# Optimization experiments

Hardware: AMD Instinct MI355X
Metric: run time of the kernel (lower is better)

Reference implementation:

```python
import jax, jax.numpy as jnp
import numpy as np
import math

T, B, H, L = 512, 64, 512, 2
STDV = 1.0 / math.sqrt(H)


def setup_inputs() -> dict:
    key = jax.random.key(0)
    ks = jax.random.split(key, 16)
    u = lambda k, shape: jax.random.uniform(k, shape, jnp.float32, -STDV, STDV)
    inp = {
        "x": jax.random.normal(ks[0], (T, B, H), jnp.float32),
        "init_states": jax.random.normal(ks[1], (L, B, H), jnp.float32),
        # stacked per-layer GRU cell parameters (input_size == hidden_size)
        "w_ir": u(ks[2], (L, H, H)), "w_hr": u(ks[3], (L, H, H)),
        "w_iz": u(ks[4], (L, H, H)), "w_hz": u(ks[5], (L, H, H)),
        "w_in": u(ks[6], (L, H, H)), "w_hn": u(ks[7], (L, H, H)),
        "b_ir": u(ks[8], (L, H)), "b_hr": u(ks[9], (L, H)),
        "b_iz": u(ks[10], (L, H)), "b_hz": u(ks[11], (L, H)),
        "b_in": u(ks[12], (L, H)), "b_hn": u(ks[13], (L, H)),
    }
    return inp


def _gru_layer(inputs, h0, w_ir, w_hr, w_iz, w_hz, w_in, w_hn,
               b_ir, b_hr, b_iz, b_hz, b_in, b_hn):
    # inputs: [T, B, H]; h0: [B, H]
    def step(h, xt):
        r = jax.nn.sigmoid(xt @ w_ir + b_ir + h @ w_hr + b_hr)
        z = jax.nn.sigmoid(xt @ w_iz + b_iz + h @ w_hz + b_hz)
        n = jnp.tanh(xt @ w_in + b_in + r * (h @ w_hn + b_hn))
        h_new = (1.0 - z) * n + z * h
        return h_new, h_new
    h_last, hs = jax.lax.scan(step, h0, inputs)
    return hs, h_last  # [T, B, H], [B, H]


def reference(x, init_states, w_ir, w_hr, w_iz, w_hz, w_in, w_hn,
              b_ir, b_hr, b_iz, b_hz, b_in, b_hn):
    num_layers = w_ir.shape[0]
    inputs = x
    finals = []
    for l in range(num_layers):
        inputs, h_last = _gru_layer(
            inputs, init_states[l],
            w_ir[l], w_hr[l], w_iz[l], w_hz[l], w_in[l], w_hn[l],
            b_ir[l], b_hr[l], b_iz[l], b_hz[l], b_in[l], b_hn[l])
        finals.append(h_last)
    # (last-layer outputs over all timesteps [T,B,H], per-layer final hidden [L,B,H])
    return inputs, jnp.stack(finals, axis=0)
```

## Files before the change

kernel.cpp:

```cpp
#include <hip/hip_runtime.h>
#include <math.h>


typedef short bf16x8 __attribute__((ext_vector_type(8)));
typedef float f32x4 __attribute__((ext_vector_type(4)));

__device__ __forceinline__ unsigned short f2bf(float f) {
  unsigned u = __builtin_bit_cast(unsigned, f);
  return (unsigned short)((u + 0x7fff + ((u >> 16) & 1)) >> 16);
}
__device__ __forceinline__ unsigned long long ldq(const unsigned long long* p) {
  return __hip_atomic_load(p, __ATOMIC_RELAXED, __HIP_MEMORY_SCOPE_AGENT);
}
__device__ __forceinline__ void stq(unsigned long long* p,
                                    unsigned long long v) {
  __hip_atomic_store(p, v, __ATOMIC_RELAXED, __HIP_MEMORY_SCOPE_AGENT);
}

__device__ __forceinline__ int hchunk(int k, int b) {
  return ((b >> 4) * 16 + (k >> 5)) * 64 + ((k >> 3) & 3) * 16 + (b & 15);
}

__device__ __forceinline__ void grid_barrier(unsigned* bar, unsigned target) {
  __syncthreads();
  if (threadIdx.x == 0) {
    unsigned leaf = blockIdx.x & 7u;
    unsigned prev = __hip_atomic_fetch_add(bar + leaf * 32, 1u,
                                           __ATOMIC_RELAXED,
                                           __HIP_MEMORY_SCOPE_AGENT);
    bool done = false;
    if ((prev & 15u) == 15u) {
      unsigned p2 = __hip_atomic_fetch_add(bar + 256, 1u, __ATOMIC_RELAXED,
                                           __HIP_MEMORY_SCOPE_AGENT);
      if ((p2 & 7u) == 7u) {
        __hip_atomic_store(bar + 288, target, __ATOMIC_RELAXED,
                           __HIP_MEMORY_SCOPE_AGENT);
        done = true;
      }
    }
    if (!done) {
      while (__hip_atomic_load(bar + 288, __ATOMIC_RELAXED,
                               __HIP_MEMORY_SCOPE_AGENT) < target) {
        __builtin_amdgcn_s_sleep(1);
      }
    }
  }
  __syncthreads();
}

__global__ void gru_prep_h(const float* __restrict__ init,
                           unsigned short* __restrict__ h0buf,
                           unsigned short* __restrict__ h1buf,
                           unsigned* __restrict__ bar) {
  int l = blockIdx.x >> 6;
  int idx = (blockIdx.x & 63) * 512 + threadIdx.x;
  int k = idx >> 6, b = idx & 63;
  unsigned short v = f2bf(init[(size_t)l * 32768 + b * 512 + k]);
  unsigned short* dst = (l == 0) ? h0buf : h1buf;
  dst[hchunk(k, b) * 8 + (k & 7)] = v;
  if (blockIdx.x == 0 && threadIdx.x < 512) bar[threadIdx.x] = 0u;
}

__global__ void gru_xprep(const float* __restrict__ x,
                          unsigned short* __restrict__ xbf) {
  int t = blockIdx.x;
#pragma unroll
  for (int it = 0; it < 8; ++it) {
    int ck = it * 512 + threadIdx.x;
    int b = (ck >> 10) * 16 + (ck & 15);
    int k0 = ((ck >> 6) & 15) * 32 + ((ck >> 4) & 3) * 8;
    const float* src = x + ((size_t)t * 64 + b) * 512 + k0;
    float4 v0 = *(const float4*)(src);
    float4 v1 = *(const float4*)(src + 4);
    unsigned short o[8] = {f2bf(v0.x), f2bf(v0.y), f2bf(v0.z), f2bf(v0.w),
                           f2bf(v1.x), f2bf(v1.y), f2bf(v1.z), f2bf(v1.w)};
    *(uint4*)(xbf + (size_t)t * 32768 + ck * 8) = *(const uint4*)o;
  }
}

__global__ void gru_wimg(const float* __restrict__ Wir,
                         const float* __restrict__ Wiz,
                         const float* __restrict__ Win,
                         const float* __restrict__ Whr,
                         const float* __restrict__ Whz,
                         const float* __restrict__ Whn,
                         unsigned short* __restrict__ wX,
                         unsigned short* __restrict__ wH) {
  int l = blockIdx.x >> 6, blk = blockIdx.x & 63;
  size_t base = ((size_t)l * 64 + blk) * 32 * 512;
  size_t wbase = (size_t)l * 512 * 512;
  for (int idx = threadIdx.x; idx < 16384; idx += 256) {
    int c = idx & 7, k = (idx >> 3) & 511, q = idx >> 12;
    int col = blk * 8 + c;
    int row = c * 4 + q;
    size_t we = wbase + (size_t)k * 512 + col;
    float vx = 0.f, vh = 0.f;
    if (q == 0) { vx = Wir[we]; vh = Whr[we]; }
    else if (q == 1) { vx = Wiz[we]; vh = Whz[we]; }
    else if (q == 2) { vx = Win[we]; }
    else { vh = Whn[we]; }
    wX[base + (size_t)row * 512 + k] = f2bf(vx);
    wH[base + (size_t)row * 512 + k] = f2bf(vh);
  }
}

__global__ __launch_bounds__(512, 1) void gru_recur_fused(
    const unsigned short* __restrict__ xbf,
    const unsigned short* __restrict__ wX,
    const unsigned short* __restrict__ wH,
    const float* __restrict__ bir, const float* __restrict__ bhr,
    const float* __restrict__ biz, const float* __restrict__ bhz,
    const float* __restrict__ bin_, const float* __restrict__ bhn,
    const float* __restrict__ init,
    unsigned short* h0buf, unsigned short* h1buf,
    float* __restrict__ Yout, float* __restrict__ finals, unsigned* bar) {
  __shared__ float ghp[2][32][66];
  __shared__ unsigned short hpack[64 * 8];
  const int tid = threadIdx.x;
  const int lane = tid & 63;
  const int wv = tid >> 6;
  const int Nt = wv & 3, Kh = wv >> 2;
  const int quad = lane >> 4, mm = lane & 15;
  const int role = blockIdx.x >> 6;
  const int blk = blockIdx.x & 63;
  const int cg0 = blk * 8;
  const int c = wv, bb = lane;
  const int cg = cg0 + c;
  const float bR = bir[role * 512 + cg] + bhr[role * 512 + cg];
  const float bZ = biz[role * 512 + cg] + bhz[role * 512 + cg];
  const float bNX = bin_[role * 512 + cg];
  const float bNH = bhn[role * 512 + cg];

  bf16x8 aX0[8], aX1[8], aH0[8], aH1[8];
  {
    const unsigned short* wXb = wX + ((size_t)role * 64 + blk) * 32 * 512;
    const unsigned short* wHb = wH + ((size_t)role * 64 + blk) * 32 * 512;
#pragma unroll
    for (int j = 0; j < 8; ++j) {
      int ko = (Kh * 8 + j) * 32 + quad * 8;
      aX0[j] = *(const bf16x8*)(wXb + (size_t)mm * 512 + ko);
      aX1[j] = *(const bf16x8*)(wXb + (size_t)(16 + mm) * 512 + ko);
      aH0[j] = *(const bf16x8*)(wHb + (size_t)mm * 512 + ko);
      aH1[j] = *(const bf16x8*)(wHb + (size_t)(16 + mm) * 512 + ko);
    }
  }
  float hp = init[(size_t)role * 32768 + bb * 512 + cg];

  for (int s = 0; s <= 512; ++s) {
    const bool active = (role == 0) ? (s < 512) : (s >= 1);
    if (active) {
      const int t = (role == 0) ? s : s - 1;
      const unsigned long long* Xq =
          (const unsigned long long*)((role == 0)
                                          ? (xbf + (size_t)t * 32768)
                                          : (h0buf + (size_t)(s & 1) * 32768));
      const unsigned long long* Hq =
          (const unsigned long long*)((role == 0)
                                          ? (h0buf + (size_t)(s & 1) * 32768)
                                          : (h1buf + (size_t)(t & 1) * 32768));
      unsigned short* Hdst = (role == 0)
                                 ? (h0buf + (size_t)((s + 1) & 1) * 32768)
                                 : (h1buf + (size_t)((t + 1) & 1) * 32768);
      unsigned long long xq[16], hq[16];
#pragma unroll
      for (int j = 0; j < 8; ++j) {
        int base = ((Nt * 16 + Kh * 8 + j) * 64 + lane) << 1;
        if (role == 0) {
          xq[2 * j] = Xq[base];
          xq[2 * j + 1] = Xq[base + 1];
        } else {
          xq[2 * j] = ldq(Xq + base);
          xq[2 * j + 1] = ldq(Xq + base + 1);
        }
        hq[2 * j] = ldq(Hq + base);
        hq[2 * j + 1] = ldq(Hq + base + 1);
      }
      f32x4 a0x = {0.f, 0.f, 0.f, 0.f}, a0h = {0.f, 0.f, 0.f, 0.f};
      f32x4 a1x = {0.f, 0.f, 0.f, 0.f}, a1h = {0.f, 0.f, 0.f, 0.f};
#pragma unroll
      for (int j = 0; j < 8; ++j) {
        union { unsigned long long q[2]; bf16x8 v; } ux, uh;
        ux.q[0] = xq[2 * j]; ux.q[1] = xq[2 * j + 1];
        uh.q[0] = hq[2 * j]; uh.q[1] = hq[2 * j + 1];
        a0x = __builtin_amdgcn_mfma_f32_16x16x32_bf16(aX0[j], ux.v, a0x, 0, 0, 0);
        a1x = __builtin_amdgcn_mfma_f32_16x16x32_bf16(aX1[j], ux.v, a1x, 0, 0, 0);
        a0h = __builtin_amdgcn_mfma_f32_16x16x32_bf16(aH0[j], uh.v, a0h, 0, 0, 0);
        a1h = __builtin_amdgcn_mfma_f32_16x16x32_bf16(aH1[j], uh.v, a1h, 0, 0, 0);
      }
      f32x4 acc0 = a0x + a0h, acc1 = a1x + a1h;
      {
        float* g = &ghp[Kh][0][0];
        int ncol = Nt * 16 + mm;
#pragma unroll
        for (int r = 0; r < 4; ++r) g[(quad * 4 + r) * 66 + ncol] = acc0[r];
#pragma unroll
        for (int r = 0; r < 4; ++r)
          g[(16 + quad * 4 + r) * 66 + ncol] = acc1[r];
      }
      __syncthreads();
      {
        float gr = ghp[0][c * 4 + 0][bb] + ghp[1][c * 4 + 0][bb];
        float gz = ghp[0][c * 4 + 1][bb] + ghp[1][c * 4 + 1][bb];
        float gnx = ghp[0][c * 4 + 2][bb] + ghp[1][c * 4 + 2][bb];
        float gnh = ghp[0][c * 4 + 3][bb] + ghp[1][c * 4 + 3][bb];
        float r = 1.0f / (1.0f + expf(-(gr + bR)));
        float z = 1.0f / (1.0f + expf(-(gz + bZ)));
        float n = tanhf(gnx + bNX + r * (gnh + bNH));
        float hnew = (1.0f - z) * n + z * hp;
        hp = hnew;
        hpack[bb * 8 + c] = f2bf(hnew);
        if (role == 1) {
          Yout[((size_t)t * 64 + bb) * 512 + cg] = hnew;
          if (t == 511) finals[32768 + bb * 512 + cg] = hnew;
        } else if (t == 511) {
          finals[bb * 512 + cg] = hnew;
        }
      }
      __syncthreads();
      if (tid < 64) {
        int ck = ((tid >> 4) * 16 + (cg0 >> 5)) * 64 + ((cg0 >> 3) & 3) * 16 +
                 (tid & 15);
        const unsigned long long* src =
            (const unsigned long long*)(hpack + tid * 8);
        unsigned long long* dst = (unsigned long long*)(Hdst + (size_t)ck * 8);
        stq(dst, src[0]);
        stq(dst + 1, src[1]);
      }
    }
    grid_barrier(bar, (unsigned)(s + 1));
  }
}

extern "C" void kernel_launch(void* const* d_in, const int* in_sizes, int n_in,
                              void* d_out, int out_size, void* d_ws,
                              size_t ws_size, hipStream_t stream) {
  const float* x = (const float*)d_in[0];
  const float* init = (const float*)d_in[1];
  const float* w_ir = (const float*)d_in[2];
  const float* w_hr = (const float*)d_in[3];
  const float* w_iz = (const float*)d_in[4];
  const float* w_hz = (const float*)d_in[5];
  const float* w_in_ = (const float*)d_in[6];
  const float* w_hn = (const float*)d_in[7];
  const float* b_ir = (const float*)d_in[8];
  const float* b_hr = (const float*)d_in[9];
  const float* b_iz = (const float*)d_in[10];
  const float* b_hz = (const float*)d_in[11];
  const float* b_in_ = (const float*)d_in[12];
  const float* b_hn = (const float*)d_in[13];
  float* out = (float*)d_out;
  float* Y = out;
  float* finals = out + (size_t)512 * 64 * 512;

  unsigned short* xbf = (unsigned short*)d_ws;
  unsigned short* wX = xbf + (size_t)512 * 32768;
  unsigned short* wH = wX + (size_t)2 * 64 * 32 * 512;
  unsigned short* h0buf = wH + (size_t)2 * 64 * 32 * 512;
  unsigned short* h1buf = h0buf + 2 * 32768;
  unsigned* bar = (unsigned*)(h1buf + 2 * 32768);

  gru_prep_h<<<128, 512, 0, stream>>>(init, h0buf, h1buf, bar);
  gru_xprep<<<512, 512, 0, stream>>>(x, xbf);
  gru_wimg<<<128, 256, 0, stream>>>(w_ir, w_iz, w_in_, w_hr, w_hz, w_hn, wX,
                                    wH);
  gru_recur_fused<<<128, 512, 0, stream>>>(
      xbf, wX, wH, b_ir, b_hr, b_iz, b_hz, b_in_, b_hn, init, h0buf, h1buf, Y,
      finals, bar);
}
```

Measured before the change: 2.621 ms.

## Split GRU recurrence into four independent batch groups with per-group barriers

Repartitions the persistent recurrent kernel so that each group of 32 blocks owns 16 batch rows, with each block computing 32 hidden columns, instead of every block computing 8 columns for all 64 batches. The grid-wide barrier becomes a 32-block per-group barrier, since batch groups never depend on each other. Activation and hidden buffers are relaid per group, and each wave now handles a single weight image (input or hidden) over 4 M-tiles. This targets synchronization cost and cross-block traffic, at the price of more weight registers per wave and a two-phase LDS reduction.

```diff
diff --git a/kernel.cpp b/kernel.cpp
--- a/kernel.cpp
+++ b/kernel.cpp
@@ -17,29 +17,26 @@
   __hip_atomic_store(p, v, __ATOMIC_RELAXED, __HIP_MEMORY_SCOPE_AGENT);
 }
 
-__device__ __forceinline__ int hchunk(int k, int b) {
-  return ((b >> 4) * 16 + (k >> 5)) * 64 + ((k >> 3) & 3) * 16 + (b & 15);
-}
-
-__device__ __forceinline__ void grid_barrier(unsigned* bar, unsigned target) {
+
+__device__ __forceinline__ void group_barrier(unsigned* gb, int sub,
+                                              unsigned target) {
   __syncthreads();
   if (threadIdx.x == 0) {
-    unsigned leaf = blockIdx.x & 7u;
-    unsigned prev = __hip_atomic_fetch_add(bar + leaf * 32, 1u,
+    unsigned prev = __hip_atomic_fetch_add(gb + (sub >> 4) * 16, 1u,
                                            __ATOMIC_RELAXED,
                                            __HIP_MEMORY_SCOPE_AGENT);
     bool done = false;
     if ((prev & 15u) == 15u) {
-      unsigned p2 = __hip_atomic_fetch_add(bar + 256, 1u, __ATOMIC_RELAXED,
+      unsigned p2 = __hip_atomic_fetch_add(gb + 32, 1u, __ATOMIC_RELAXED,
                                            __HIP_MEMORY_SCOPE_AGENT);
-      if ((p2 & 7u) == 7u) {
-        __hip_atomic_store(bar + 288, target, __ATOMIC_RELAXED,
+      if ((p2 & 1u) == 1u) {
+        __hip_atomic_store(gb + 48, target, __ATOMIC_RELAXED,
                            __HIP_MEMORY_SCOPE_AGENT);
         done = true;
       }
     }
     if (!done) {
-      while (__hip_atomic_load(bar + 288, __ATOMIC_RELAXED,
+      while (__hip_atomic_load(gb + 48, __ATOMIC_RELAXED,
                                __HIP_MEMORY_SCOPE_AGENT) < target) {
         __builtin_amdgcn_s_sleep(1);
       }
@@ -56,8 +53,10 @@
   int idx = (blockIdx.x & 63) * 512 + threadIdx.x;
   int k = idx >> 6, b = idx & 63;
   unsigned short v = f2bf(init[(size_t)l * 32768 + b * 512 + k]);
+  int g = b >> 4;
+  int chunk = (k >> 5) * 64 + ((k >> 3) & 3) * 16 + (b & 15);
   unsigned short* dst = (l == 0) ? h0buf : h1buf;
-  dst[hchunk(k, b) * 8 + (k & 7)] = v;
+  dst[(size_t)(g * 2) * 8192 + chunk * 8 + (k & 7)] = v;
   if (blockIdx.x == 0 && threadIdx.x < 512) bar[threadIdx.x] = 0u;
 }
 
@@ -67,14 +66,16 @@
 #pragma unroll
   for (int it = 0; it < 8; ++it) {
     int ck = it * 512 + threadIdx.x;
-    int b = (ck >> 10) * 16 + (ck & 15);
-    int k0 = ((ck >> 6) & 15) * 32 + ((ck >> 4) & 3) * 8;
-    const float* src = x + ((size_t)t * 64 + b) * 512 + k0;
+    int b = ck >> 6, kc = ck & 63;
+    int g = b >> 4;
+    int chunk = (kc >> 2) * 64 + (kc & 3) * 16 + (b & 15);
+    const float* src = x + ((size_t)t * 64 + b) * 512 + kc * 8;
     float4 v0 = *(const float4*)(src);
     float4 v1 = *(const float4*)(src + 4);
     unsigned short o[8] = {f2bf(v0.x), f2bf(v0.y), f2bf(v0.z), f2bf(v0.w),
                            f2bf(v1.x), f2bf(v1.y), f2bf(v1.z), f2bf(v1.w)};
-    *(uint4*)(xbf + (size_t)t * 32768 + ck * 8) = *(const uint4*)o;
+    *(uint4*)(xbf + ((size_t)t * 4 + g) * 8192 + chunk * 8) =
+        *(const uint4*)o;
   }
 }
 
@@ -86,12 +87,13 @@
                          const float* __restrict__ Whn,
                          unsigned short* __restrict__ wX,
                          unsigned short* __restrict__ wH) {
-  int l = blockIdx.x >> 6, blk = blockIdx.x & 63;
-  size_t base = ((size_t)l * 64 + blk) * 32 * 512;
+  int l = blockIdx.x >> 6, sub = blockIdx.x & 63;
+  int cb = sub >> 2, q = sub & 3;
+  size_t base = ((size_t)l * 16 + cb) * 128 * 512;
   size_t wbase = (size_t)l * 512 * 512;
   for (int idx = threadIdx.x; idx < 16384; idx += 256) {
-    int c = idx & 7, k = (idx >> 3) & 511, q = idx >> 12;
-    int col = blk * 8 + c;
+    int k = idx >> 5, c = idx & 31;
+    int col = cb * 32 + c;
     int row = c * 4 + q;
     size_t we = wbase + (size_t)k * 512 + col;
     float vx = 0.f, vh = 0.f;
@@ -112,122 +114,143 @@
     const float* __restrict__ biz, const float* __restrict__ bhz,
     const float* __restrict__ bin_, const float* __restrict__ bhn,
     const float* __restrict__ init,
-    unsigned short* h0buf, unsigned short* h1buf,
+    unsigned short* h0buf,
+    unsigned short* h1buf,
     float* __restrict__ Yout, float* __restrict__ finals, unsigned* bar) {
-  __shared__ float ghp[2][32][66];
+  __shared__ float ghp[2][128][17];
   __shared__ unsigned short hpack[64 * 8];
   const int tid = threadIdx.x;
   const int lane = tid & 63;
   const int wv = tid >> 6;
-  const int Nt = wv & 3, Kh = wv >> 2;
+  const int Kh = wv & 1, mh = (wv >> 1) & 1, img = wv >> 2;
   const int quad = lane >> 4, mm = lane & 15;
-  const int role = blockIdx.x >> 6;
-  const int blk = blockIdx.x & 63;
-  const int cg0 = blk * 8;
-  const int c = wv, bb = lane;
-  const int cg = cg0 + c;
+  const int g = blockIdx.x >> 5;
+  const int sub = blockIdx.x & 31;
+  const int role = sub >> 4;
+  const int blk = sub & 15;
+  const int eb = tid & 15, ec = tid >> 4;
+  const int cg = blk * 32 + ec;
+  const int bbg = g * 16 + eb;
   const float bR = bir[role * 512 + cg] + bhr[role * 512 + cg];
   const float bZ = biz[role * 512 + cg] + bhz[role * 512 + cg];
   const float bNX = bin_[role * 512 + cg];
   const float bNH = bhn[role * 512 + cg];
-
-  bf16x8 aX0[8], aX1[8], aH0[8], aH1[8];
+  unsigned* gb = bar + g * 64;
+
+  bf16x8 a[4][8];
   {
-    const unsigned short* wXb = wX + ((size_t)role * 64 + blk) * 32 * 512;
-    const unsigned short* wHb = wH + ((size_t)role * 64 + blk) * 32 * 512;
-#pragma unroll
-    for (int j = 0; j < 8; ++j) {
-      int ko = (Kh * 8 + j) * 32 + quad * 8;
-      aX0[j] = *(const bf16x8*)(wXb + (size_t)mm * 512 + ko);
-      aX1[j] = *(const bf16x8*)(wXb + (size_t)(16 + mm) * 512 + ko);
-      aH0[j] = *(const bf16x8*)(wHb + (size_t)mm * 512 + ko);
-      aH1[j] = *(const bf16x8*)(wHb + (size_t)(16 + mm) * 512 + ko);
-    }
-  }
-  float hp = init[(size_t)role * 32768 + bb * 512 + cg];
+    const unsigned short* wIb =
+        (img == 0 ? wX : wH) + ((size_t)role * 16 + blk) * 65536;
+#pragma unroll
+    for (int mt = 0; mt < 4; ++mt)
+#pragma unroll
+      for (int j = 0; j < 8; ++j) {
+        int row = mh * 64 + mt * 16 + mm;
+        int ko = (Kh * 8 + j) * 32 + quad * 8;
+        a[mt][j] = *(const bf16x8*)(wIb + (size_t)row * 512 + ko);
+      }
+  }
+  float hp = init[(size_t)role * 32768 + (size_t)bbg * 512 + cg];
 
   for (int s = 0; s <= 512; ++s) {
     const bool active = (role == 0) ? (s < 512) : (s >= 1);
     if (active) {
       const int t = (role == 0) ? s : s - 1;
-      const unsigned long long* Xq =
-          (const unsigned long long*)((role == 0)
-                                          ? (xbf + (size_t)t * 32768)
-                                          : (h0buf + (size_t)(s & 1) * 32768));
-      const unsigned long long* Hq =
-          (const unsigned long long*)((role == 0)
-                                          ? (h0buf + (size_t)(s & 1) * 32768)
-                                          : (h1buf + (size_t)(t & 1) * 32768));
-      unsigned short* Hdst = (role == 0)
-                                 ? (h0buf + (size_t)((s + 1) & 1) * 32768)
-                                 : (h1buf + (size_t)((t + 1) & 1) * 32768);
-      unsigned long long xq[16], hq[16];
+      const unsigned long long* Bq;
+      bool atomicB;
+      if (role == 0) {
+        if (img == 0) {
+          Bq = (const unsigned long long*)(xbf + ((size_t)t * 4 + g) * 8192);
+          atomicB = false;
+        } else {
+          Bq = (const unsigned long long*)(h0buf +
+                                           ((size_t)g * 2 + (s & 1)) * 8192);
+          atomicB = true;
+        }
+      } else {
+        if (img == 0) {
+          Bq = (const unsigned long long*)(h0buf +
+                                           ((size_t)g * 2 + (s & 1)) * 8192);
+        } else {
+          Bq = (const unsigned long long*)(h1buf +
+                                           ((size_t)g * 2 + (t & 1)) * 8192);
+        }
+        atomicB = true;
+      }
+      unsigned short* Hdst =
+          (role == 0) ? (h0buf + ((size_t)g * 2 + ((s + 1) & 1)) * 8192)
+                      : (h1buf + ((size_t)g * 2 + ((t + 1) & 1)) * 8192);
+      unsigned long long bq[16];
 #pragma unroll
       for (int j = 0; j < 8; ++j) {
-        int base = ((Nt * 16 + Kh * 8 + j) * 64 + lane) << 1;
-        if (role == 0) {
-          xq[2 * j] = Xq[base];
-          xq[2 * j + 1] = Xq[base + 1];
+        int base = ((Kh * 8 + j) * 64 + lane) << 1;
+        if (atomicB) {
+          bq[2 * j] = ldq(Bq + base);
+          bq[2 * j + 1] = ldq(Bq + base + 1);
         } else {
-          xq[2 * j] = ldq(Xq + base);
-          xq[2 * j + 1] = ldq(Xq + base + 1);
-        }
-        hq[2 * j] = ldq(Hq + base);
-        hq[2 * j + 1] = ldq(Hq + base + 1);
-      }
-      f32x4 a0x = {0.f, 0.f, 0.f, 0.f}, a0h = {0.f, 0.f, 0.f, 0.f};
-      f32x4 a1x = {0.f, 0.f, 0.f, 0.f}, a1h = {0.f, 0.f, 0.f, 0.f};
+          bq[2 * j] = Bq[base];
+          bq[2 * j + 1] = Bq[base + 1];
+        }
+      }
+      f32x4 acc[4];
+#pragma unroll
+      for (int mt = 0; mt < 4; ++mt) acc[mt] = {0.f, 0.f, 0.f, 0.f};
 #pragma unroll
       for (int j = 0; j < 8; ++j) {
-        union { unsigned long long q[2]; bf16x8 v; } ux, uh;
-        ux.q[0] = xq[2 * j]; ux.q[1] = xq[2 * j + 1];
-        uh.q[0] = hq[2 * j]; uh.q[1] = hq[2 * j + 1];
-        a0x = __builtin_amdgcn_mfma_f32_16x16x32_bf16(aX0[j], ux.v, a0x, 0, 0, 0);
-        a1x = __builtin_amdgcn_mfma_f32_16x16x32_bf16(aX1[j], ux.v, a1x, 0, 0, 0);
-        a0h = __builtin_amdgcn_mfma_f32_16x16x32_bf16(aH0[j], uh.v, a0h, 0, 0, 0);
-        a1h = __builtin_amdgcn_mfma_f32_16x16x32_bf16(aH1[j], uh.v, a1h, 0, 0, 0);
-      }
-      f32x4 acc0 = a0x + a0h, acc1 = a1x + a1h;
-      {
-        float* g = &ghp[Kh][0][0];
-        int ncol = Nt * 16 + mm;
-#pragma unroll
-        for (int r = 0; r < 4; ++r) g[(quad * 4 + r) * 66 + ncol] = acc0[r];
-#pragma unroll
-        for (int r = 0; r < 4; ++r)
-          g[(16 + quad * 4 + r) * 66 + ncol] = acc1[r];
+        union { unsigned long long q[2]; bf16x8 v; } ub;
+        ub.q[0] = bq[2 * j];
+        ub.q[1] = bq[2 * j + 1];
+#pragma unroll
+        for (int mt = 0; mt < 4; ++mt)
+          acc[mt] =
+              __builtin_amdgcn_mfma_f32_16x16x32_bf16(a[mt][j], ub.v, acc[mt],
+                                                      0, 0, 0);
+      }
+      if (Kh == 0) {
+#pragma unroll
+        for (int mt = 0; mt < 4; ++mt)
+#pragma unroll
+          for (int r = 0; r < 4; ++r)
+            ghp[img][mh * 64 + mt * 16 + quad * 4 + r][mm] = acc[mt][r];
+      }
+      __syncthreads();
+      if (Kh == 1) {
+#pragma unroll
+        for (int mt = 0; mt < 4; ++mt)
+#pragma unroll
+          for (int r = 0; r < 4; ++r)
+            ghp[img][mh * 64 + mt * 16 + quad * 4 + r][mm] += acc[mt][r];
       }
       __syncthreads();
       {
-        float gr = ghp[0][c * 4 + 0][bb] + ghp[1][c * 4 + 0][bb];
-        float gz = ghp[0][c * 4 + 1][bb] + ghp[1][c * 4 + 1][bb];
-        float gnx = ghp[0][c * 4 + 2][bb] + ghp[1][c * 4 + 2][bb];
-        float gnh = ghp[0][c * 4 + 3][bb] + ghp[1][c * 4 + 3][bb];
+        float gr = ghp[0][ec * 4 + 0][eb] + ghp[1][ec * 4 + 0][eb];
+        float gz = ghp[0][ec * 4 + 1][eb] + ghp[1][ec * 4 + 1][eb];
+        float gnx = ghp[0][ec * 4 + 2][eb] + ghp[1][ec * 4 + 2][eb];
+        float gnh = ghp[0][ec * 4 + 3][eb] + ghp[1][ec * 4 + 3][eb];
         float r = 1.0f / (1.0f + expf(-(gr + bR)));
         float z = 1.0f / (1.0f + expf(-(gz + bZ)));
         float n = tanhf(gnx + bNX + r * (gnh + bNH));
         float hnew = (1.0f - z) * n + z * hp;
         hp = hnew;
-        hpack[bb * 8 + c] = f2bf(hnew);
+        hpack[(((ec >> 3) & 3) * 16 + eb) * 8 + (ec & 7)] = f2bf(hnew);
         if (role == 1) {
-          Yout[((size_t)t * 64 + bb) * 512 + cg] = hnew;
-          if (t == 511) finals[32768 + bb * 512 + cg] = hnew;
+          Yout[((size_t)t * 64 + bbg) * 512 + cg] = hnew;
+          if (t == 511) finals[32768 + (size_t)bbg * 512 + cg] = hnew;
         } else if (t == 511) {
-          finals[bb * 512 + cg] = hnew;
+          finals[(size_t)bbg * 512 + cg] = hnew;
         }
       }
       __syncthreads();
-      if (tid < 64) {
-        int ck = ((tid >> 4) * 16 + (cg0 >> 5)) * 64 + ((cg0 >> 3) & 3) * 16 +
-                 (tid & 15);
+      if (wv == 0) {
         const unsigned long long* src =
-            (const unsigned long long*)(hpack + tid * 8);
-        unsigned long long* dst = (unsigned long long*)(Hdst + (size_t)ck * 8);
+            (const unsigned long long*)(hpack + lane * 8);
+        unsigned long long* dst =
+            (unsigned long long*)(Hdst + ((size_t)blk * 64 + lane) * 8);
         stq(dst, src[0]);
         stq(dst + 1, src[1]);
       }
     }
-    grid_barrier(bar, (unsigned)(s + 1));
+    group_barrier(gb, sub, (unsigned)(s + 1));
   }
 }
 
@@ -254,10 +277,10 @@
 
   unsigned short* xbf = (unsigned short*)d_ws;
   unsigned short* wX = xbf + (size_t)512 * 32768;
-  unsigned short* wH = wX + (size_t)2 * 64 * 32 * 512;
-  unsigned short* h0buf = wH + (size_t)2 * 64 * 32 * 512;
-  unsigned short* h1buf = h0buf + 2 * 32768;
-  unsigned* bar = (unsigned*)(h1buf + 2 * 32768);
+  unsigned short* wH = wX + (size_t)2 * 16 * 128 * 512;
+  unsigned short* h0buf = wH + (size_t)2 * 16 * 128 * 512;
+  unsigned short* h1buf = h0buf + (size_t)4 * 2 * 8192;
+  unsigned* bar = (unsigned*)(h1buf + (size_t)4 * 2 * 8192);
 
   gru_prep_h<<<128, 512, 0, stream>>>(init, h0buf, h1buf, bar);
   gru_xprep<<<512, 512, 0, stream>>>(x, xbf);
```

Result: slower. 3.180 ms (+21.4%).

## Decouple GRU layers with per-layer barriers and a 4-deep h0 ring buffer

Applied to the files above, without the earlier changes.

The single grid barrier across all 128 blocks is replaced by two independent 64-block barriers, one per layer. Layer 1 now waits on layer 0's generation counter before consuming its output, and layer 0 waits on layer 1 before overwriting a slot. The layer-0 hidden-state buffer becomes a 4-slot ring so the two layers can drift apart without a lockstep global sync. Layer 1's Yout store is deferred by one step so it overlaps the wait. In exchange, the code adds cross-layer spin-waits and extra workspace for the ring.

```diff
diff --git a/kernel.cpp b/kernel.cpp
--- a/kernel.cpp
+++ b/kernel.cpp
@@ -16,33 +16,33 @@
                                     unsigned long long v) {
   __hip_atomic_store(p, v, __ATOMIC_RELAXED, __HIP_MEMORY_SCOPE_AGENT);
 }
+__device__ __forceinline__ unsigned ldw(const unsigned* p) {
+  return __hip_atomic_load(p, __ATOMIC_RELAXED, __HIP_MEMORY_SCOPE_AGENT);
+}
 
 __device__ __forceinline__ int hchunk(int k, int b) {
   return ((b >> 4) * 16 + (k >> 5)) * 64 + ((k >> 3) & 3) * 16 + (b & 15);
 }
 
-__device__ __forceinline__ void grid_barrier(unsigned* bar, unsigned target) {
+__device__ __forceinline__ void layer_barrier(unsigned* rb, int blk,
+                                              unsigned target) {
   __syncthreads();
   if (threadIdx.x == 0) {
-    unsigned leaf = blockIdx.x & 7u;
-    unsigned prev = __hip_atomic_fetch_add(bar + leaf * 32, 1u,
+    unsigned prev = __hip_atomic_fetch_add(rb + (blk & 7) * 16, 1u,
                                            __ATOMIC_RELAXED,
                                            __HIP_MEMORY_SCOPE_AGENT);
     bool done = false;
-    if ((prev & 15u) == 15u) {
-      unsigned p2 = __hip_atomic_fetch_add(bar + 256, 1u, __ATOMIC_RELAXED,
+    if ((prev & 7u) == 7u) {
+      unsigned p2 = __hip_atomic_fetch_add(rb + 128, 1u, __ATOMIC_RELAXED,
                                            __HIP_MEMORY_SCOPE_AGENT);
       if ((p2 & 7u) == 7u) {
-        __hip_atomic_store(bar + 288, target, __ATOMIC_RELAXED,
+        __hip_atomic_store(rb + 144, target, __ATOMIC_RELAXED,
                            __HIP_MEMORY_SCOPE_AGENT);
         done = true;
       }
     }
     if (!done) {
-      while (__hip_atomic_load(bar + 288, __ATOMIC_RELAXED,
-                               __HIP_MEMORY_SCOPE_AGENT) < target) {
-        __builtin_amdgcn_s_sleep(1);
-      }
+      while (ldw(rb + 144) < target) __builtin_amdgcn_s_sleep(1);
     }
   }
   __syncthreads();
@@ -112,7 +112,8 @@
     const float* __restrict__ biz, const float* __restrict__ bhz,
     const float* __restrict__ bin_, const float* __restrict__ bhn,
     const float* __restrict__ init,
-    unsigned short* h0buf, unsigned short* h1buf,
+    unsigned short* h0buf,
+    unsigned short* h1buf,
     float* __restrict__ Yout, float* __restrict__ finals, unsigned* bar) {
   __shared__ float ghp[2][32][66];
   __shared__ unsigned short hpack[64 * 8];
@@ -130,6 +131,9 @@
   const float bZ = biz[role * 512 + cg] + bhz[role * 512 + cg];
   const float bNX = bin_[role * 512 + cg];
   const float bNH = bhn[role * 512 + cg];
+  unsigned* rb = bar + role * 256;
+  const unsigned* gen0 = bar + 144;
+  const unsigned* gen1 = bar + 256 + 144;
 
   bf16x8 aX0[8], aX1[8], aH0[8], aH1[8];
   {
@@ -146,88 +150,96 @@
   }
   float hp = init[(size_t)role * 32768 + bb * 512 + cg];
 
-  for (int s = 0; s <= 512; ++s) {
-    const bool active = (role == 0) ? (s < 512) : (s >= 1);
-    if (active) {
-      const int t = (role == 0) ? s : s - 1;
-      const unsigned long long* Xq =
-          (const unsigned long long*)((role == 0)
-                                          ? (xbf + (size_t)t * 32768)
-                                          : (h0buf + (size_t)(s & 1) * 32768));
-      const unsigned long long* Hq =
-          (const unsigned long long*)((role == 0)
-                                          ? (h0buf + (size_t)(s & 1) * 32768)
-                                          : (h1buf + (size_t)(t & 1) * 32768));
-      unsigned short* Hdst = (role == 0)
-                                 ? (h0buf + (size_t)((s + 1) & 1) * 32768)
-                                 : (h1buf + (size_t)((t + 1) & 1) * 32768);
-      unsigned long long xq[16], hq[16];
-#pragma unroll
-      for (int j = 0; j < 8; ++j) {
-        int base = ((Nt * 16 + Kh * 8 + j) * 64 + lane) << 1;
-        if (role == 0) {
-          xq[2 * j] = Xq[base];
-          xq[2 * j + 1] = Xq[base + 1];
-        } else {
-          xq[2 * j] = ldq(Xq + base);
-          xq[2 * j + 1] = ldq(Xq + base + 1);
-        }
-        hq[2 * j] = ldq(Hq + base);
-        hq[2 * j + 1] = ldq(Hq + base + 1);
-      }
-      f32x4 a0x = {0.f, 0.f, 0.f, 0.f}, a0h = {0.f, 0.f, 0.f, 0.f};
-      f32x4 a1x = {0.f, 0.f, 0.f, 0.f}, a1h = {0.f, 0.f, 0.f, 0.f};
-#pragma unroll
-      for (int j = 0; j < 8; ++j) {
-        union { unsigned long long q[2]; bf16x8 v; } ux, uh;
-        ux.q[0] = xq[2 * j]; ux.q[1] = xq[2 * j + 1];
-        uh.q[0] = hq[2 * j]; uh.q[1] = hq[2 * j + 1];
-        a0x = __builtin_amdgcn_mfma_f32_16x16x32_bf16(aX0[j], ux.v, a0x, 0, 0, 0);
-        a1x = __builtin_amdgcn_mfma_f32_16x16x32_bf16(aX1[j], ux.v, a1x, 0, 0, 0);
-        a0h = __builtin_amdgcn_mfma_f32_16x16x32_bf16(aH0[j], uh.v, a0h, 0, 0, 0);
-        a1h = __builtin_amdgcn_mfma_f32_16x16x32_bf16(aH1[j], uh.v, a1h, 0, 0, 0);
-      }
-      f32x4 acc0 = a0x + a0h, acc1 = a1x + a1h;
-      {
-        float* g = &ghp[Kh][0][0];
-        int ncol = Nt * 16 + mm;
-#pragma unroll
-        for (int r = 0; r < 4; ++r) g[(quad * 4 + r) * 66 + ncol] = acc0[r];
-#pragma unroll
-        for (int r = 0; r < 4; ++r)
-          g[(16 + quad * 4 + r) * 66 + ncol] = acc1[r];
+  const int sBeg = (role == 0) ? 0 : 1;
+  const int sEnd = (role == 0) ? 511 : 512;
+  for (int s = sBeg; s <= sEnd; ++s) {
+    const int t = (role == 0) ? s : s - 1;
+    if (role == 1) {
+      if (s >= 2) Yout[((size_t)(s - 2) * 64 + bb) * 512 + cg] = hp;
+      if (tid == 0) {
+        while (ldw(gen0) < (unsigned)s) __builtin_amdgcn_s_sleep(1);
       }
       __syncthreads();
-      {
-        float gr = ghp[0][c * 4 + 0][bb] + ghp[1][c * 4 + 0][bb];
-        float gz = ghp[0][c * 4 + 1][bb] + ghp[1][c * 4 + 1][bb];
-        float gnx = ghp[0][c * 4 + 2][bb] + ghp[1][c * 4 + 2][bb];
-        float gnh = ghp[0][c * 4 + 3][bb] + ghp[1][c * 4 + 3][bb];
-        float r = 1.0f / (1.0f + expf(-(gr + bR)));
-        float z = 1.0f / (1.0f + expf(-(gz + bZ)));
-        float n = tanhf(gnx + bNX + r * (gnh + bNH));
-        float hnew = (1.0f - z) * n + z * hp;
-        hp = hnew;
-        hpack[bb * 8 + c] = f2bf(hnew);
-        if (role == 1) {
-          Yout[((size_t)t * 64 + bb) * 512 + cg] = hnew;
-          if (t == 511) finals[32768 + bb * 512 + cg] = hnew;
-        } else if (t == 511) {
-          finals[bb * 512 + cg] = hnew;
-        }
-      }
-      __syncthreads();
-      if (tid < 64) {
-        int ck = ((tid >> 4) * 16 + (cg0 >> 5)) * 64 + ((cg0 >> 3) & 3) * 16 +
-                 (tid & 15);
-        const unsigned long long* src =
-            (const unsigned long long*)(hpack + tid * 8);
-        unsigned long long* dst = (unsigned long long*)(Hdst + (size_t)ck * 8);
-        stq(dst, src[0]);
-        stq(dst + 1, src[1]);
-      }
-    }
-    grid_barrier(bar, (unsigned)(s + 1));
+    }
+    const unsigned long long* Xq =
+        (const unsigned long long*)((role == 0)
+                                        ? (xbf + (size_t)t * 32768)
+                                        : (h0buf + (size_t)(s & 3) * 32768));
+    const unsigned long long* Hq =
+        (const unsigned long long*)((role == 0)
+                                        ? (h0buf + (size_t)(s & 3) * 32768)
+                                        : (h1buf + (size_t)(t & 1) * 32768));
+    unsigned short* Hdst = (role == 0)
+                               ? (h0buf + (size_t)((s + 1) & 3) * 32768)
+                               : (h1buf + (size_t)((t + 1) & 1) * 32768);
+    unsigned long long xq[16], hq[16];
+#pragma unroll
+    for (int j = 0; j < 8; ++j) {
+      int base = ((Nt * 16 + Kh * 8 + j) * 64 + lane) << 1;
+      if (role == 0) {
+        xq[2 * j] = Xq[base];
+        xq[2 * j + 1] = Xq[base + 1];
+      } else {
+        xq[2 * j] = ldq(Xq + base);
+        xq[2 * j + 1] = ldq(Xq + base + 1);
+      }
+      hq[2 * j] = ldq(Hq + base);
+      hq[2 * j + 1] = ldq(Hq + base + 1);
+    }
+    f32x4 a0x = {0.f, 0.f, 0.f, 0.f}, a0h = {0.f, 0.f, 0.f, 0.f};
+    f32x4 a1x = {0.f, 0.f, 0.f, 0.f}, a1h = {0.f, 0.f, 0.f, 0.f};
+#pragma unroll
+    for (int j = 0; j < 8; ++j) {
+      union { unsigned long long q[2]; bf16x8 v; } ux, uh;
+      ux.q[0] = xq[2 * j]; ux.q[1] = xq[2 * j + 1];
+      uh.q[0] = hq[2 * j]; uh.q[1] = hq[2 * j + 1];
+      a0x = __builtin_amdgcn_mfma_f32_16x16x32_bf16(aX0[j], ux.v, a0x, 0, 0, 0);
+      a1x = __builtin_amdgcn_mfma_f32_16x16x32_bf16(aX1[j], ux.v, a1x, 0, 0, 0);
+      a0h = __builtin_amdgcn_mfma_f32_16x16x32_bf16(aH0[j], uh.v, a0h, 0, 0, 0);
+      a1h = __builtin_amdgcn_mfma_f32_16x16x32_bf16(aH1[j], uh.v, a1h, 0, 0, 0);
+    }
+    f32x4 acc0 = a0x + a0h, acc1 = a1x + a1h;
+    {
+      float* g = &ghp[Kh][0][0];
+      int ncol = Nt * 16 + mm;
+#pragma unroll
+      for (int r = 0; r < 4; ++r) g[(quad * 4 + r) * 66 + ncol] = acc0[r];
+#pragma unroll
+      for (int r = 0; r < 4; ++r)
+        g[(16 + quad * 4 + r) * 66 + ncol] = acc1[r];
+    }
+    __syncthreads();
+    {
+      float gr = ghp[0][c * 4 + 0][bb] + ghp[1][c * 4 + 0][bb];
+      float gz = ghp[0][c * 4 + 1][bb] + ghp[1][c * 4 + 1][bb];
+      float gnx = ghp[0][c * 4 + 2][bb] + ghp[1][c * 4 + 2][bb];
+      float gnh = ghp[0][c * 4 + 3][bb] + ghp[1][c * 4 + 3][bb];
+      float r = 1.0f / (1.0f + expf(-(gr + bR)));
+      float z = 1.0f / (1.0f + expf(-(gz + bZ)));
+      float n = tanhf(gnx + bNX + r * (gnh + bNH));
+      float hnew = (1.0f - z) * n + z * hp;
+      hp = hnew;
+      hpack[bb * 8 + c] = f2bf(hnew);
+      if (role == 0 && t == 511) finals[bb * 512 + cg] = hnew;
+    }
+    __syncthreads();
+    if (tid < 64) {
+      if (role == 0 && s >= 3) {
+        while (ldw(gen1) < (unsigned)(s - 2)) __builtin_amdgcn_s_sleep(1);
+      }
+      int ck = ((tid >> 4) * 16 + (cg0 >> 5)) * 64 + ((cg0 >> 3) & 3) * 16 +
+               (tid & 15);
+      const unsigned long long* src =
+          (const unsigned long long*)(hpack + tid * 8);
+      unsigned long long* dst = (unsigned long long*)(Hdst + (size_t)ck * 8);
+      stq(dst, src[0]);
+      stq(dst + 1, src[1]);
+    }
+    layer_barrier(rb, blk, (unsigned)(s + 1));
+  }
+  if (role == 1) {
+    Yout[((size_t)511 * 64 + bb) * 512 + cg] = hp;
+    finals[32768 + bb * 512 + cg] = hp;
   }
 }
 
@@ -256,7 +268,7 @@
   unsigned short* wX = xbf + (size_t)512 * 32768;
   unsigned short* wH = wX + (size_t)2 * 64 * 32 * 512;
   unsigned short* h0buf = wH + (size_t)2 * 64 * 32 * 512;
-  unsigned short* h1buf = h0buf + 2 * 32768;
+  unsigned short* h1buf = h0buf + (size_t)4 * 32768;
   unsigned* bar = (unsigned*)(h1buf + 2 * 32768);
 
   gru_prep_h<<<128, 512, 0, stream>>>(init, h0buf, h1buf, bar);
```

Measured after the change: 3.394 ms. +29.5%, slower.
